# Kernel optimization log

Hardware: AMD Instinct MI355X
Metric: run time of the kernel (lower is better)

The kernel has to match this reference:

```python
import jax, jax.numpy as jnp
import numpy as np

B, N, D, H, M, CD = 2, 2048, 1024, 16, 77, 768
DH = D // H          # head dim 64
FF = 4 * D           # GEGLU hidden 4096
NBITS = 8
EPS = 1e-5


def fake_quant_w(w, n_bits=NBITS):
    """Per-tensor uniform affine INT8 fake-quant (UniformAffineQuantizerINT8) with STE."""
    levels = 2 ** n_bits - 1
    mn = jnp.min(w)
    mx = jnp.max(w)
    delta = (mx - mn) / levels
    zp = jnp.round(-mn / delta)
    wq = jnp.clip(jnp.round(w / delta) + zp, 0, levels)
    wdq = (wq - zp) * delta
    return w + jax.lax.stop_gradient(wdq - w)


def layernorm(x, g, b):
    mu = jnp.mean(x, axis=-1, keepdims=True)
    var = jnp.mean((x - mu) ** 2, axis=-1, keepdims=True)
    return (x - mu) * jax.lax.rsqrt(var + EPS) * g + b


def linear(x, w, b=None):
    y = x @ fake_quant_w(w).T
    return y if b is None else y + b


def cross_attn(x, ctx, qw, kw, vw, ow, ob):
    Bq, Nq, _ = x.shape
    Nk = ctx.shape[1]
    q = linear(x, qw).reshape(Bq, Nq, H, DH)     # b n h d
    k = linear(ctx, kw).reshape(Bq, Nk, H, DH)
    v = linear(ctx, vw).reshape(Bq, Nk, H, DH)
    scale = DH ** -0.5
    sim = jnp.einsum('bihd,bjhd->bhij', q, k) * scale   # [B,H,Nq,Nk]
    attn = jax.nn.softmax(sim, axis=-1)
    out = jnp.einsum('bhij,bjhd->bihd', attn, v).reshape(Bq, Nq, D)
    return linear(out, ow, ob)


def geglu_ff(x, w1, b1, w2, b2):
    h = linear(x, w1, b1)                # [B,N,2*FF]
    hidden, gate = jnp.split(h, 2, axis=-1)
    return linear(hidden * jax.nn.gelu(gate), w2, b2)


def setup_inputs() -> dict:
    key = jax.random.key(0)
    ks = jax.random.split(key, 24)
    W = lambda k, o, i: (jax.random.normal(k, (o, i), jnp.float32) * 0.02)
    return {
        'x': jax.random.normal(ks[0], (B, N, D), jnp.float32),
        'context': jax.random.normal(ks[1], (B, M, CD), jnp.float32),
        'ln1_g': 1.0 + 0.1 * jax.random.normal(ks[2], (D,), jnp.float32),
        'ln1_b': 0.1 * jax.random.normal(ks[3], (D,), jnp.float32),
        'ln2_g': 1.0 + 0.1 * jax.random.normal(ks[4], (D,), jnp.float32),
        'ln2_b': 0.1 * jax.random.normal(ks[5], (D,), jnp.float32),
        'ln3_g': 1.0 + 0.1 * jax.random.normal(ks[6], (D,), jnp.float32),
        'ln3_b': 0.1 * jax.random.normal(ks[7], (D,), jnp.float32),
        'q1_w': W(ks[8], D, D), 'k1_w': W(ks[9], D, D), 'v1_w': W(ks[10], D, D),
        'o1_w': W(ks[11], D, D), 'o1_b': jnp.zeros((D,), jnp.float32),
        'q2_w': W(ks[12], D, D), 'k2_w': W(ks[13], D, CD), 'v2_w': W(ks[14], D, CD),
        'o2_w': W(ks[15], D, D), 'o2_b': jnp.zeros((D,), jnp.float32),
        'ff1_w': W(ks[16], 2 * FF, D), 'ff1_b': jnp.zeros((2 * FF,), jnp.float32),
        'ff2_w': W(ks[17], D, FF), 'ff2_b': jnp.zeros((D,), jnp.float32),
    }


def reference(x, context, ln1_g, ln1_b, ln2_g, ln2_b, ln3_g, ln3_b,
              q1_w, k1_w, v1_w, o1_w, o1_b,
              q2_w, k2_w, v2_w, o2_w, o2_b,
              ff1_w, ff1_b, ff2_w, ff2_b):
    x = cross_attn(layernorm(x, ln1_g, ln1_b), layernorm(x, ln1_g, ln1_b),
                   q1_w, k1_w, v1_w, o1_w, o1_b) + x
    x = cross_attn(layernorm(x, ln2_g, ln2_b), context,
                   q2_w, k2_w, v2_w, o2_w, o2_b) + x
    x = geglu_ff(layernorm(x, ln3_g, ln3_b), ff1_w, ff1_b, ff2_w, ff2_b) + x
    return x
```

## Files before the change

### kernel.cpp

```cpp
#include <hip/hip_runtime.h>
#include <cstdint>
#include <cstddef>

typedef unsigned short ushort_t;
typedef short s16x8 __attribute__((ext_vector_type(8)));
typedef float f32x4 __attribute__((ext_vector_type(4)));
typedef unsigned u32x4 __attribute__((ext_vector_type(4)));

#define MFMA(A,B,C) __builtin_amdgcn_mfma_f32_16x16x32_bf16((A),(B),(C),0,0,0)

__device__ __forceinline__ float b2f(ushort_t h){ return __uint_as_float(((unsigned)h)<<16); }
__device__ __forceinline__ ushort_t f2b(float f){
  unsigned u = __float_as_uint(f);
  u += 0x7FFFu + ((u >> 16) & 1u);
  return (ushort_t)(u >> 16);
}
__device__ __forceinline__ unsigned f2o(float f){
  unsigned u = __float_as_uint(f);
  return (u & 0x80000000u) ? ~u : (u | 0x80000000u);
}
__device__ __forceinline__ float o2f(unsigned u){
  unsigned b = (u & 0x80000000u) ? (u & 0x7FFFFFFFu) : ~u;
  return __uint_as_float(b);
}

struct QT { const float* w[10]; ushort_t* o[10]; int n[10]; float os[10]; int pm[10]; };

__global__ void init_k(unsigned* slots){
  int t = threadIdx.x;
  if (t < 20) slots[t] = (t & 1) ? 0u : 0xFFFFFFFFu;
}

__global__ __launch_bounds__(256) void minmax_k(QT qt, unsigned* slots){
  int t = blockIdx.y;
  const float4* w = (const float4*)qt.w[t];
  int n4 = qt.n[t] >> 2;
  float mn = 3.4e38f, mx = -3.4e38f;
  for (int i = blockIdx.x*256 + threadIdx.x; i < n4; i += gridDim.x*256){
    float4 v = w[i];
    mn = fminf(mn, fminf(fminf(v.x, v.y), fminf(v.z, v.w)));
    mx = fmaxf(mx, fmaxf(fmaxf(v.x, v.y), fmaxf(v.z, v.w)));
  }
  #pragma unroll
  for (int o = 1; o < 64; o <<= 1){
    mn = fminf(mn, __shfl_xor(mn, o));
    mx = fmaxf(mx, __shfl_xor(mx, o));
  }
  __shared__ float smn[4], smx[4];
  int wv = threadIdx.x >> 6;
  if ((threadIdx.x & 63) == 0){ smn[wv] = mn; smx[wv] = mx; }
  __syncthreads();
  if (threadIdx.x == 0){
    mn = fminf(fminf(smn[0], smn[1]), fminf(smn[2], smn[3]));
    mx = fmaxf(fmaxf(smx[0], smx[1]), fmaxf(smx[2], smx[3]));
    atomicMin(&slots[2*t], f2o(mn));
    atomicMax(&slots[2*t+1], f2o(mx));
  }
}

__global__ __launch_bounds__(256) void dequant_k(QT qt, const unsigned* __restrict__ slots){
  int t = blockIdx.y;
  float mn = o2f(slots[2*t]), mx = o2f(slots[2*t+1]);
  float delta = (mx - mn) * (1.f/255.f);
  float zp = rintf(-mn / delta);
  float osc = qt.os[t];
  int pm = qt.pm[t];
  const float4* w = (const float4*)qt.w[t];
  ushort4* o = (ushort4*)qt.o[t];
  int n4 = qt.n[t] >> 2;
  for (int i = blockIdx.x*256 + threadIdx.x; i < n4; i += gridDim.x*256){
    float4 v = w[i];
    ushort4 r;
    float q;
    q = fminf(fmaxf(rintf(v.x/delta) + zp, 0.f), 255.f); r.x = f2b((q - zp)*delta*osc);
    q = fminf(fmaxf(rintf(v.y/delta) + zp, 0.f), 255.f); r.y = f2b((q - zp)*delta*osc);
    q = fminf(fmaxf(rintf(v.z/delta) + zp, 0.f), 255.f); r.z = f2b((q - zp)*delta*osc);
    q = fminf(fmaxf(rintf(v.w/delta) + zp, 0.f), 255.f); r.w = f2b((q - zp)*delta*osc);
    size_t oi = i;
    if (pm){
      int row = i >> 8, c4 = i & 255;
      int nr = (row < 4096) ? ((row >> 5) << 6) + (row & 31)
                            : (((row - 4096) >> 5) << 6) + 32 + ((row - 4096) & 31);
      oi = (size_t)nr*256 + c4;
    }
    o[oi] = r;
  }
}

__global__ __launch_bounds__(256) void f2b_k(const float* __restrict__ in, ushort_t* __restrict__ out, int n4){
  for (int i = blockIdx.x*256 + threadIdx.x; i < n4; i += gridDim.x*256){
    float4 v = ((const float4*)in)[i];
    ushort4 r; r.x = f2b(v.x); r.y = f2b(v.y); r.z = f2b(v.z); r.w = f2b(v.w);
    ((ushort4*)out)[i] = r;
  }
}

__global__ __launch_bounds__(256) void ln_k(const float* __restrict__ x, const float* __restrict__ g,
                                            const float* __restrict__ b, ushort_t* __restrict__ out){
  int row = blockIdx.x, tid = threadIdx.x;
  float4 v = ((const float4*)(x + (size_t)row*1024))[tid];
  float s  = v.x + v.y + v.z + v.w;
  float s2 = v.x*v.x + v.y*v.y + v.z*v.z + v.w*v.w;
  #pragma unroll
  for (int o = 1; o < 64; o <<= 1){ s += __shfl_xor(s, o); s2 += __shfl_xor(s2, o); }
  __shared__ float rs[4], rs2[4];
  int wv = tid >> 6;
  if ((tid & 63) == 0){ rs[wv] = s; rs2[wv] = s2; }
  __syncthreads();
  s = rs[0]+rs[1]+rs[2]+rs[3]; s2 = rs2[0]+rs2[1]+rs2[2]+rs2[3];
  float mu = s * (1.f/1024.f);
  float var = s2 * (1.f/1024.f) - mu*mu;
  float rstd = rsqrtf(var + 1e-5f);
  float4 gv = ((const float4*)g)[tid], bv = ((const float4*)b)[tid];
  ushort4 r;
  r.x = f2b((v.x - mu)*rstd*gv.x + bv.x);
  r.y = f2b((v.y - mu)*rstd*gv.y + bv.y);
  r.z = f2b((v.z - mu)*rstd*gv.z + bv.z);
  r.w = f2b((v.w - mu)*rstd*gv.w + bv.w);
  ((ushort4*)(out + (size_t)row*1024))[tid] = r;
}

__global__ __launch_bounds__(256) void reduce_ln_k(
    const float* __restrict__ p0, const float* __restrict__ p1,
    const float* __restrict__ bias, const float* __restrict__ resid,
    const float* __restrict__ lng, const float* __restrict__ lnb_,
    float* __restrict__ xout, ushort_t* __restrict__ lnout)
{
  int row = blockIdx.x, tid = threadIdx.x;
  size_t bi = (size_t)row*256 + tid;
  float4 a = ((const float4*)p0)[bi];
  float4 b = ((const float4*)p1)[bi];
  float4 r = ((const float4*)resid)[bi];
  float4 bb = ((const float4*)bias)[tid];
  float4 v;
  v.x = a.x + b.x + r.x + bb.x;
  v.y = a.y + b.y + r.y + bb.y;
  v.z = a.z + b.z + r.z + bb.z;
  v.w = a.w + b.w + r.w + bb.w;
  ((float4*)xout)[bi] = v;
  float s  = v.x + v.y + v.z + v.w;
  float s2 = v.x*v.x + v.y*v.y + v.z*v.z + v.w*v.w;
  #pragma unroll
  for (int o = 1; o < 64; o <<= 1){ s += __shfl_xor(s, o); s2 += __shfl_xor(s2, o); }
  __shared__ float rs[4], rs2[4];
  int wv = tid >> 6;
  if ((tid & 63) == 0){ rs[wv] = s; rs2[wv] = s2; }
  __syncthreads();
  s = rs[0]+rs[1]+rs[2]+rs[3]; s2 = rs2[0]+rs2[1]+rs2[2]+rs2[3];
  float mu = s * (1.f/1024.f);
  float var = s2 * (1.f/1024.f) - mu*mu;
  float rstd = rsqrtf(var + 1e-5f);
  float4 gv = ((const float4*)lng)[tid], bv = ((const float4*)lnb_)[tid];
  ushort4 o;
  o.x = f2b((v.x - mu)*rstd*gv.x + bv.x);
  o.y = f2b((v.y - mu)*rstd*gv.y + bv.y);
  o.z = f2b((v.z - mu)*rstd*gv.z + bv.z);
  o.w = f2b((v.w - mu)*rstd*gv.w + bv.w);
  ((ushort4*)(lnout + (size_t)row*1024))[tid] = o;
}

__global__ __launch_bounds__(512) void gemm_k(
    const ushort_t* __restrict__ A, const ushort_t* __restrict__ W,
    const float* __restrict__ bias, const float* __restrict__ resid,
    float* __restrict__ outF, ushort_t* __restrict__ outB,
    int M, int N, int K, int lda, int ldw)
{
  __shared__ ushort_t As[3][256*32];
  __shared__ ushort_t Bs[3][128*32];
  const int tid = threadIdx.x;
  const int lane = tid & 63, wv = tid >> 6;
  const int g = lane >> 4, qi = lane & 15;

  const int gx = gridDim.x, gy = gridDim.y;
  const int lid = blockIdx.x + blockIdx.y * gx;
  int m0, n0;
  if (((gx & 3) | (gy & 1)) == 0){
    const int w = gx >> 2, h = gy >> 1;
    const int xcd = lid & 7, o = lid >> 3;
    const int cx = xcd & 3, cy = xcd >> 2;
    n0 = (cx * w + (o % w)) * 128;
    m0 = (cy * h + (o / w)) * 256;
  } else {
    n0 = blockIdx.x * 128;
    m0 = blockIdx.y * 256;
  }

  const int koff = blockIdx.z * K;
  if (gridDim.z > 1) outF += (size_t)blockIdx.z * M * N;

  const int wr = (wv >> 1) * 64, wc = (wv & 1) * 64;
  f32x4 acc[4][4] = {};

  const int ra0 = tid >> 2,        sa0 = (tid & 3) ^ ((ra0 >> 1) & 3);
  const int ra1 = (512+tid) >> 2,  sa1 = ((512+tid) & 3) ^ ((ra1 >> 1) & 3);
  const int aA0 = (m0 + ra0 < M) ? m0 + ra0 : M - 1;
  const int aA1 = (m0 + ra1 < M) ? m0 + ra1 : M - 1;
  const size_t dA0 = (size_t)tid*8, dA1 = (size_t)(512+tid)*8, dB0 = (size_t)tid*8;

  #define GSTAGE(bi_, kt_) do {                                                    \
    __builtin_amdgcn_global_load_lds(                                              \
      (const __attribute__((address_space(1))) void*)(A + (size_t)aA0*lda + koff + (kt_) + sa0*8), \
      (__attribute__((address_space(3))) void*)(&As[bi_][dA0]), 16, 0, 0);         \
    __builtin_amdgcn_global_load_lds(                                              \
      (const __attribute__((address_space(1))) void*)(A + (size_t)aA1*lda + koff + (kt_) + sa1*8), \
      (__attribute__((address_space(3))) void*)(&As[bi_][dA1]), 16, 0, 0);         \
    __builtin_amdgcn_global_load_lds(                                              \
      (const __attribute__((address_space(1))) void*)(W + (size_t)(n0 + ra0)*ldw + koff + (kt_) + sa0*8), \
      (__attribute__((address_space(3))) void*)(&Bs[bi_][dB0]), 16, 0, 0);         \
  } while(0)

  const int nt = K >> 5;
  GSTAGE(0, 0);
  if (nt > 1) GSTAGE(1, 32);
  if (nt > 1) asm volatile("s_waitcnt vmcnt(3)" ::: "memory");
  else        asm volatile("s_waitcnt vmcnt(0)" ::: "memory");
  __builtin_amdgcn_s_barrier();
  __builtin_amdgcn_sched_barrier(0);

  int bi = 0;
  for (int t = 0; t < nt; ++t){
    int b2 = bi + 2; if (b2 >= 3) b2 -= 3;
    if (t + 2 < nt) GSTAGE(b2, (t + 2) << 5);
    s16x8 af[4], bfr[4];
    #pragma unroll
    for (int mi = 0; mi < 4; ++mi){
      int row = wr + mi*16 + qi;
      int sl = g ^ ((row >> 1) & 3);
      af[mi] = *(const s16x8*)(&As[bi][row*32 + sl*8]);
    }
    #pragma unroll
    for (int ni = 0; ni < 4; ++ni){
      int row = wc + ni*16 + qi;
      int sl = g ^ ((row >> 1) & 3);
      bfr[ni] = *(const s16x8*)(&Bs[bi][row*32 + sl*8]);
    }
    __builtin_amdgcn_s_setprio(1);
    #pragma unroll
    for (int mi = 0; mi < 4; ++mi)
      #pragma unroll
      for (int ni = 0; ni < 4; ++ni)
        acc[mi][ni] = MFMA(af[mi], bfr[ni], acc[mi][ni]);
    __builtin_amdgcn_s_setprio(0);
    if (t + 1 < nt){
      if (t + 2 < nt) asm volatile("s_waitcnt vmcnt(3)" ::: "memory");
      else            asm volatile("s_waitcnt vmcnt(0)" ::: "memory");
      __builtin_amdgcn_s_barrier();
      __builtin_amdgcn_sched_barrier(0);
    }
    bi += 1; if (bi >= 3) bi -= 3;
  }
  #undef GSTAGE

  #pragma unroll
  for (int mi = 0; mi < 4; ++mi){
    #pragma unroll
    for (int r = 0; r < 4; ++r){
      int row = m0 + wr + mi*16 + g*4 + r;
      if (row >= M) continue;
      #pragma unroll
      for (int ni = 0; ni < 4; ++ni){
        int col = n0 + wc + ni*16 + qi;
        float v = acc[mi][ni][r];
        if (bias)  v += bias[col];
        if (resid) v += resid[(size_t)row*N + col];
        if (outF)  outF[(size_t)row*N + col] = v;
        else       outB[(size_t)row*N + col] = f2b(v);
      }
    }
  }
}

__global__ __launch_bounds__(512) void gemm_ff1_k(
    const ushort_t* __restrict__ A, const ushort_t* __restrict__ W,
    const float* __restrict__ biasHG, ushort_t* __restrict__ out)
{
  __shared__ ushort_t As[3][256*32];
  __shared__ ushort_t Bs[3][128*32];
  const int tid = threadIdx.x;
  const int lane = tid & 63, wv = tid >> 6;
  const int g = lane >> 4, qi = lane & 15;
  const int lda = 1024, ldw = 1024;

  const int gx = gridDim.x;
  const int gy = gridDim.y;
  const int lid = blockIdx.x + blockIdx.y * gx;
  const int w = gx >> 2, h = gy >> 1;
  const int xcd = lid & 7, o = lid >> 3;
  const int cx = xcd & 3, cy = xcd >> 2;
  const int n0 = (cx * w + (o % w)) * 128;
  const int m0 = (cy * h + (o / w)) * 256;

  const int wr = (wv >> 1) * 64, wc = (wv & 1) * 64;
  f32x4 acc[4][4] = {};

  const int ra0 = tid >> 2,        sa0 = (tid & 3) ^ ((ra0 >> 1) & 3);
  const int ra1 = (512+tid) >> 2,  sa1 = ((512+tid) & 3) ^ ((ra1 >> 1) & 3);
  const int aA0 = m0 + ra0, aA1 = m0 + ra1;
  const size_t dA0 = (size_t)tid*8, dA1 = (size_t)(512+tid)*8, dB0 = (size_t)tid*8;

  #define GSTAGEF(bi_, kt_) do {                                                   \
    __builtin_amdgcn_global_load_lds(                                              \
      (const __attribute__((address_space(1))) void*)(A + (size_t)aA0*lda + (kt_) + sa0*8), \
      (__attribute__((address_space(3))) void*)(&As[bi_][dA0]), 16, 0, 0);         \
    __builtin_amdgcn_global_load_lds(                                              \
      (const __attribute__((address_space(1))) void*)(A + (size_t)aA1*lda + (kt_) + sa1*8), \
      (__attribute__((address_space(3))) void*)(&As[bi_][dA1]), 16, 0, 0);         \
    __builtin_amdgcn_global_load_lds(                                              \
      (const __attribute__((address_space(1))) void*)(W + (size_t)(n0 + ra0)*ldw + (kt_) + sa0*8), \
      (__attribute__((address_space(3))) void*)(&Bs[bi_][dB0]), 16, 0, 0);         \
  } while(0)

  const int nt = 1024 >> 5;
  GSTAGEF(0, 0);
  GSTAGEF(1, 32);
  asm volatile("s_waitcnt vmcnt(3)" ::: "memory");
  __builtin_amdgcn_s_barrier();
  __builtin_amdgcn_sched_barrier(0);

  int bi = 0;
  for (int t = 0; t < nt; ++t){
    int b2 = bi + 2; if (b2 >= 3) b2 -= 3;
    if (t + 2 < nt) GSTAGEF(b2, (t + 2) << 5);
    s16x8 af[4], bfr[4];
    #pragma unroll
    for (int mi = 0; mi < 4; ++mi){
      int row = wr + mi*16 + qi;
      int sl = g ^ ((row >> 1) & 3);
      af[mi] = *(const s16x8*)(&As[bi][row*32 + sl*8]);
    }
    #pragma unroll
    for (int ni = 0; ni < 4; ++ni){
      int row = wc + ni*16 + qi;
      int sl = g ^ ((row >> 1) & 3);
      bfr[ni] = *(const s16x8*)(&Bs[bi][row*32 + sl*8]);
    }
    __builtin_amdgcn_s_setprio(1);
    #pragma unroll
    for (int mi = 0; mi < 4; ++mi)
      #pragma unroll
      for (int ni = 0; ni < 4; ++ni)
        acc[mi][ni] = MFMA(af[mi], bfr[ni], acc[mi][ni]);
    __builtin_amdgcn_s_setprio(0);
    if (t + 1 < nt){
      if (t + 2 < nt) asm volatile("s_waitcnt vmcnt(3)" ::: "memory");
      else            asm volatile("s_waitcnt vmcnt(0)" ::: "memory");
      __builtin_amdgcn_s_barrier();
      __builtin_amdgcn_sched_barrier(0);
    }
    bi += 1; if (bi >= 3) bi -= 3;
  }
  #undef GSTAGEF

  const int jw = (n0 + wc) >> 1;
  #pragma unroll
  for (int mi = 0; mi < 4; ++mi){
    #pragma unroll
    for (int r = 0; r < 4; ++r){
      int row = m0 + wr + mi*16 + g*4 + r;
      #pragma unroll
      for (int ni = 0; ni < 2; ++ni){
        int j = jw + ni*16 + qi;
        float hv = acc[mi][ni][r]   + biasHG[j];
        float gg = acc[mi][ni+2][r] + biasHG[4096 + j];
        float tt = 0.7978845608f*(gg + 0.044715f*gg*gg*gg);
        float e  = __builtin_amdgcn_exp2f(2.885390082f*tt);
        float th = 1.f - 2.f/(e + 1.f);
        float ge = 0.5f*gg*(1.f + th);
        out[(size_t)row*4096 + j] = f2b(hv * ge);
      }
    }
  }
}

__global__ __launch_bounds__(256) void reduce_k(const float* __restrict__ p0, const float* __restrict__ p1,
                                                const float* __restrict__ bias, const float* __restrict__ resid,
                                                float* __restrict__ outF, ushort_t* __restrict__ outB, int n4){
  for (int i = blockIdx.x*256 + threadIdx.x; i < n4; i += gridDim.x*256){
    float4 a = ((const float4*)p0)[i];
    float4 b = ((const float4*)p1)[i];
    float4 v;
    v.x = a.x + b.x; v.y = a.y + b.y; v.z = a.z + b.z; v.w = a.w + b.w;
    if (bias){
      float4 bb = ((const float4*)bias)[i & 255];
      v.x += bb.x; v.y += bb.y; v.z += bb.z; v.w += bb.w;
    }
    if (resid){
      float4 r = ((const float4*)resid)[i];
      v.x += r.x; v.y += r.y; v.z += r.z; v.w += r.w;
    }
    if (outF) ((float4*)outF)[i] = v;
    else {
      ushort4 o; o.x = f2b(v.x); o.y = f2b(v.y); o.z = f2b(v.z); o.w = f2b(v.w);
      ((ushort4*)outB)[i] = o;
    }
  }
}

__global__ __launch_bounds__(256) void reduce4_k(const float* __restrict__ p0, const float* __restrict__ p1,
                                                 const float* __restrict__ p2, const float* __restrict__ p3,
                                                 const float* __restrict__ bias, const float* __restrict__ resid,
                                                 float* __restrict__ outF, int n4){
  for (int i = blockIdx.x*256 + threadIdx.x; i < n4; i += gridDim.x*256){
    float4 a = ((const float4*)p0)[i];
    float4 b = ((const float4*)p1)[i];
    float4 c = ((const float4*)p2)[i];
    float4 d = ((const float4*)p3)[i];
    float4 r = ((const float4*)resid)[i];
    float4 bb = ((const float4*)bias)[i & 255];
    float4 v;
    v.x = (a.x + b.x) + (c.x + d.x) + r.x + bb.x;
    v.y = (a.y + b.y) + (c.y + d.y) + r.y + bb.y;
    v.z = (a.z + b.z) + (c.z + d.z) + r.z + bb.z;
    v.w = (a.w + b.w) + (c.w + d.w) + r.w + bb.w;
    ((float4*)outF)[i] = v;
  }
}

__global__ __launch_bounds__(256) void vtrans_k(const ushort_t* __restrict__ src, ushort_t* __restrict__ dst,
                                                int rows, int stride, int col_off, int nk_pad){
  __shared__ ushort_t ldst[64*130];
  int n0 = blockIdx.x * 128;
  int b = blockIdx.y >> 4, h = blockIdx.y & 15;
  const ushort_t* s = src + (size_t)b*rows*stride + col_off + h*64;
  for (int idx = threadIdx.x; idx < 128*64; idx += 256){
    int n = idx >> 6, d = idx & 63;
    int ng = n0 + n;
    ushort_t v = (ng < rows) ? s[(size_t)ng*stride + d] : (ushort_t)0;
    ldst[d*130 + n] = v;
  }
  __syncthreads();
  ushort_t* o = dst + (size_t)(b*16 + h)*64*nk_pad;
  for (int idx = threadIdx.x; idx < 64*128; idx += 256){
    int d = idx >> 7, n = idx & 127;
    if (n0 + n < nk_pad) o[(size_t)d*nk_pad + n0 + n] = ldst[d*130 + n];
  }
}

__global__ __launch_bounds__(512) void attn_k(
    const ushort_t* __restrict__ Q, const ushort_t* __restrict__ Kp, const ushort_t* __restrict__ Vt,
    ushort_t* __restrict__ O, int nq, int nk, int qstride, int kvstride, int nk_pad)
{
  __shared__ ushort_t Ks[2][32*64];
  __shared__ ushort_t Vs[2][64*32];
  const int tid = threadIdx.x, lane = tid & 63, wv = tid >> 6;
  const int g = lane >> 4, qi = lane & 15;
  const int b = blockIdx.y >> 4, h = blockIdx.y & 15;
  const int q0 = blockIdx.x*128 + wv*16;

  const ushort_t* Qr = Q + (size_t)(b*nq + q0 + qi)*qstride + h*64;
  s16x8 qf0 = *(const s16x8*)(Qr + g*8);
  s16x8 qf1 = *(const s16x8*)(Qr + 32 + g*8);
  const ushort_t* Kb = Kp + (size_t)b*nk*kvstride + h*64;
  const ushort_t* Vb = Vt + (size_t)(b*16 + h)*64*nk_pad;

  const int krow = (wv & 3)*8 + (lane >> 3);
  const int kgsl = (lane & 7) ^ (krow & 7);
  const int vrow = (wv & 3)*16 + (lane >> 2);
  const int vgsl = (lane & 3) ^ ((vrow >> 1) & 3);

  #define STAGE(buf, kb_) do {                                                   \
    if (wv < 4){                                                                 \
      int kr_ = (kb_) + krow; if (kr_ >= nk) kr_ = nk - 1;                       \
      __builtin_amdgcn_global_load_lds(                                          \
        (const __attribute__((address_space(1))) void*)(Kb + (size_t)kr_*kvstride + kgsl*8), \
        (__attribute__((address_space(3))) void*)(&Ks[buf][(size_t)(wv&3)*512]), 16, 0, 0); \
    } else {                                                                     \
      __builtin_amdgcn_global_load_lds(                                          \
        (const __attribute__((address_space(1))) void*)(Vb + (size_t)vrow*nk_pad + (kb_) + vgsl*8), \
        (__attribute__((address_space(3))) void*)(&Vs[buf][(size_t)(wv&3)*512]), 16, 0, 0); \
    }                                                                            \
  } while(0)

  const int nkp = (nk + 31) & ~31;
  f32x4 ot[4] = {};
  float m_run = -1e30f, lsum = 0.f;

  const int ks0 = (g     ^ (qi & 7)) * 8;
  const int ks1 = ((4+g) ^ (qi & 7)) * 8;
  const int vs0 = (g ^ ((qi >> 1) & 3)) * 8;

  STAGE(0, 0);
  asm volatile("s_waitcnt vmcnt(0)" ::: "memory");
  __syncthreads();
  int cur = 0;
  for (int kb = 0; kb < nkp; kb += 32){
    if (kb + 32 < nkp) STAGE(cur^1, kb + 32);
    s16x8 ka0 = *(const s16x8*)(&Ks[cur][(qi)*64      + ks0]);
    s16x8 ka1 = *(const s16x8*)(&Ks[cur][(qi)*64      + ks1]);
    s16x8 kb0 = *(const s16x8*)(&Ks[cur][(16+qi)*64   + ks0]);
    s16x8 kb1 = *(const s16x8*)(&Ks[cur][(16+qi)*64   + ks1]);
    s16x8 vf0 = *(const s16x8*)(&Vs[cur][(qi)*32      + vs0]);
    s16x8 vf1 = *(const s16x8*)(&Vs[cur][(16+qi)*32   + vs0]);
    s16x8 vf2 = *(const s16x8*)(&Vs[cur][(32+qi)*32   + vs0]);
    s16x8 vf3 = *(const s16x8*)(&Vs[cur][(48+qi)*32   + vs0]);

    f32x4 st0 = {}, st1 = {};
    __builtin_amdgcn_s_setprio(1);
    st0 = MFMA(ka0, qf0, st0);
    st0 = MFMA(ka1, qf1, st0);
    st1 = MFMA(kb0, qf0, st1);
    st1 = MFMA(kb1, qf1, st1);
    __builtin_amdgcn_s_setprio(0);
    float s[8];
    #pragma unroll
    for (int r = 0; r < 4; ++r){ s[r] = st0[r]; s[4+r] = st1[r]; }
    if (kb + 32 > nk){
      #pragma unroll
      for (int r = 0; r < 4; ++r){
        if (kb + 4*g + r >= nk)      s[r]   = -1e30f;
        if (kb + 16 + 4*g + r >= nk) s[4+r] = -1e30f;
      }
    }
    float m1 = fmaxf(fmaxf(s[0], s[1]), s[2]);
    float m2 = fmaxf(fmaxf(s[3], s[4]), s[5]);
    float bm = fmaxf(fmaxf(m1, m2), fmaxf(s[6], s[7]));
    bm = fmaxf(bm, __shfl_xor(bm, 16));
    bm = fmaxf(bm, __shfl_xor(bm, 32));
    if (!__all(bm <= m_run)){
      float m_new = fmaxf(m_run, bm);
      float fac = __builtin_amdgcn_exp2f(m_run - m_new);
      lsum *= fac;
      #pragma unroll
      for (int dd = 0; dd < 4; ++dd)
        #pragma unroll
        for (int r = 0; r < 4; ++r) ot[dd][r] *= fac;
      m_run = m_new;
    }
    float p[8], ps = 0.f;
    #pragma unroll
    for (int i = 0; i < 8; ++i){ p[i] = __builtin_amdgcn_exp2f(s[i] - m_run); ps += p[i]; }
    lsum += ps;
    unsigned pk[4];
    #pragma unroll
    for (int r = 0; r < 4; ++r)
      asm("v_cvt_pk_bf16_f32 %0, %1, %2" : "=v"(pk[r]) : "v"(p[r]), "v"(p[4+r]));
    int srcbase = ((2*g) & 3) * 16 + qi;
    unsigned sh0[4], sh1[4];
    #pragma unroll
    for (int r = 0; r < 4; ++r){
      sh0[r] = (unsigned)__shfl((int)pk[r], srcbase);
      sh1[r] = (unsigned)__shfl((int)pk[r], srcbase + 16);
    }
    unsigned sel = (g >> 1) ? 0x07060302u : 0x05040100u;
    u32x4 pw;
    pw[0] = __builtin_amdgcn_perm(sh0[1], sh0[0], sel);
    pw[1] = __builtin_amdgcn_perm(sh0[3], sh0[2], sel);
    pw[2] = __builtin_amdgcn_perm(sh1[1], sh1[0], sel);
    pw[3] = __builtin_amdgcn_perm(sh1[3], sh1[2], sel);
    s16x8 pf = __builtin_bit_cast(s16x8, pw);
    __builtin_amdgcn_s_setprio(1);
    ot[0] = MFMA(vf0, pf, ot[0]);
    ot[1] = MFMA(vf1, pf, ot[1]);
    ot[2] = MFMA(vf2, pf, ot[2]);
    ot[3] = MFMA(vf3, pf, ot[3]);
    __builtin_amdgcn_s_setprio(0);

    asm volatile("s_waitcnt vmcnt(0)" ::: "memory");
    __syncthreads();
    cur ^= 1;
  }
  #undef STAGE
  float l = lsum;
  l += __shfl_xor(l, 16);
  l += __shfl_xor(l, 32);
  float inv = 1.f / l;
  ushort_t* Or = O + (size_t)(b*nq + q0 + qi)*1024 + h*64;
  #pragma unroll
  for (int dd = 0; dd < 4; ++dd)
    #pragma unroll
    for (int r = 0; r < 4; ++r)
      Or[dd*16 + 4*g + r] = f2b(ot[dd][r] * inv);
}

extern "C" void kernel_launch(void* const* d_in, const int* in_sizes, int n_in,
                              void* d_out, int out_size, void* d_ws, size_t ws_size,
                              hipStream_t stream)
{
  const float* x    = (const float*)d_in[0];
  const float* ctx  = (const float*)d_in[1];
  const float* ln1g = (const float*)d_in[2];
  const float* ln1b = (const float*)d_in[3];
  const float* ln2g = (const float*)d_in[4];
  const float* ln2b = (const float*)d_in[5];
  const float* ln3g = (const float*)d_in[6];
  const float* ln3b = (const float*)d_in[7];
  const float* q1w  = (const float*)d_in[8];
  const float* k1w  = (const float*)d_in[9];
  const float* v1w  = (const float*)d_in[10];
  const float* o1w  = (const float*)d_in[11];
  const float* o1b  = (const float*)d_in[12];
  const float* q2w  = (const float*)d_in[13];
  const float* k2w  = (const float*)d_in[14];
  const float* v2w  = (const float*)d_in[15];
  const float* o2w  = (const float*)d_in[16];
  const float* o2b  = (const float*)d_in[17];
  const float* ff1w = (const float*)d_in[18];
  const float* ff1b = (const float*)d_in[19];
  const float* ff2w = (const float*)d_in[20];
  const float* ff2b = (const float*)d_in[21];

  char* base = (char*)d_ws;
  size_t off = 0;
  auto alloc = [&](size_t bytes) -> char* {
    char* p = base + off;
    off += (bytes + 255) & ~(size_t)255;
    return p;
  };
  unsigned*  slots = (unsigned*)alloc(80);
  ushort_t*  ctxb  = (ushort_t*)alloc((size_t)154*768*2);
  ushort_t*  wqkv1 = (ushort_t*)alloc((size_t)3072*1024*2);
  ushort_t*  o1d   = (ushort_t*)alloc((size_t)1024*1024*2);
  ushort_t*  q2d   = (ushort_t*)alloc((size_t)1024*1024*2);
  ushort_t*  wkv2  = (ushort_t*)alloc((size_t)2048*768*2);
  ushort_t*  o2d   = (ushort_t*)alloc((size_t)1024*1024*2);
  ushort_t*  f1d   = (ushort_t*)alloc((size_t)8192*1024*2);
  ushort_t*  f2d   = (ushort_t*)alloc((size_t)1024*4096*2);
  ushort_t*  lnb   = (ushort_t*)alloc((size_t)4096*1024*2);
  ushort_t*  qkvb  = (ushort_t*)alloc((size_t)4096*3072*2);
  ushort_t*  q2b   = (ushort_t*)alloc((size_t)4096*1024*2);
  ushort_t*  atb   = (ushort_t*)alloc((size_t)4096*1024*2);
  ushort_t*  kvb   = (ushort_t*)alloc((size_t)154*2048*2);
  ushort_t*  vt1   = (ushort_t*)alloc((size_t)2*16*64*2048*2);
  ushort_t*  vt2   = (ushort_t*)alloc((size_t)2*16*64*96*2);
  float*     x1    = (float*)alloc((size_t)4096*1024*4);
  float*     x2    = (float*)alloc((size_t)4096*1024*4);
  ushort_t*  hb    = (ushort_t*)alloc((size_t)4096*8192*2);
  ushort_t*  actb  = qkvb;
  float*     part  = (float*)hb;
  float*     part1 = part + (size_t)4096*1024;
  float*     part2 = part + (size_t)2*4096*1024;
  float*     part3 = part + (size_t)3*4096*1024;

  const float SC = 0.18033688011f;
  QT qt;
  qt.w[0]=q1w;  qt.o[0]=wqkv1;               qt.n[0]=1024*1024; qt.os[0]=SC;  qt.pm[0]=0;
  qt.w[1]=k1w;  qt.o[1]=wqkv1+1024*1024;     qt.n[1]=1024*1024; qt.os[1]=1.f; qt.pm[1]=0;
  qt.w[2]=v1w;  qt.o[2]=wqkv1+2*1024*1024;   qt.n[2]=1024*1024; qt.os[2]=1.f; qt.pm[2]=0;
  qt.w[3]=o1w;  qt.o[3]=o1d;                 qt.n[3]=1024*1024; qt.os[3]=1.f; qt.pm[3]=0;
  qt.w[4]=q2w;  qt.o[4]=q2d;                 qt.n[4]=1024*1024; qt.os[4]=SC;  qt.pm[4]=0;
  qt.w[5]=k2w;  qt.o[5]=wkv2;                qt.n[5]=1024*768;  qt.os[5]=1.f; qt.pm[5]=0;
  qt.w[6]=v2w;  qt.o[6]=wkv2+1024*768;       qt.n[6]=1024*768;  qt.os[6]=1.f; qt.pm[6]=0;
  qt.w[7]=o2w;  qt.o[7]=o2d;                 qt.n[7]=1024*1024; qt.os[7]=1.f; qt.pm[7]=0;
  qt.w[8]=ff1w; qt.o[8]=f1d;                 qt.n[8]=8192*1024; qt.os[8]=1.f; qt.pm[8]=1;
  qt.w[9]=ff2w; qt.o[9]=f2d;                 qt.n[9]=1024*4096; qt.os[9]=1.f; qt.pm[9]=0;

  init_k<<<1, 64, 0, stream>>>(slots);
  minmax_k<<<dim3(256,10), 256, 0, stream>>>(qt, slots);
  dequant_k<<<dim3(256,10), 256, 0, stream>>>(qt, slots);
  f2b_k<<<64, 256, 0, stream>>>(ctx, ctxb, 154*768/4);

  ln_k<<<4096, 256, 0, stream>>>(x, ln1g, ln1b, lnb);
  gemm_k<<<dim3(24, 16), 512, 0, stream>>>(lnb, wqkv1, nullptr, nullptr,
                                           nullptr, qkvb, 4096, 3072, 1024, 1024, 1024);
  vtrans_k<<<dim3(16, 32), 256, 0, stream>>>(qkvb, vt1, 2048, 3072, 2048, 2048);
  attn_k<<<dim3(16, 32), 512, 0, stream>>>(qkvb, qkvb+1024, vt1, atb,
                                           2048, 2048, 3072, 3072, 2048);
  gemm_k<<<dim3(8, 16, 2), 512, 0, stream>>>(atb, o1d, nullptr, nullptr,
                                             part, nullptr, 4096, 1024, 512, 1024, 1024);
  reduce_ln_k<<<4096, 256, 0, stream>>>(part, part1, o1b, x, ln2g, ln2b, x1, lnb);

  gemm_k<<<dim3(8, 16, 2), 512, 0, stream>>>(lnb, q2d, nullptr, nullptr,
                                             part, nullptr, 4096, 1024, 512, 1024, 1024);
  reduce_k<<<2048, 256, 0, stream>>>(part, part1, nullptr, nullptr, nullptr, q2b, 4096*1024/4);
  gemm_k<<<dim3(16, 1), 512, 0, stream>>>(ctxb, wkv2, nullptr, nullptr,
                                          nullptr, kvb, 154, 2048, 768, 768, 768);
  vtrans_k<<<dim3(1, 32), 256, 0, stream>>>(kvb, vt2, 77, 2048, 1024, 96);
  attn_k<<<dim3(16, 32), 512, 0, stream>>>(q2b, kvb, vt2, atb,
                                           2048, 77, 1024, 2048, 96);
  gemm_k<<<dim3(8, 16, 2), 512, 0, stream>>>(atb, o2d, nullptr, nullptr,
                                             part, nullptr, 4096, 1024, 512, 1024, 1024);
  reduce_ln_k<<<4096, 256, 0, stream>>>(part, part1, o2b, x1, ln3g, ln3b, x2, lnb);

  gemm_ff1_k<<<dim3(64, 16), 512, 0, stream>>>(lnb, f1d, ff1b, actb);
  gemm_k<<<dim3(8, 16, 4), 512, 0, stream>>>(actb, f2d, nullptr, nullptr,
                                             part, nullptr, 4096, 1024, 1024, 4096, 4096);
  reduce4_k<<<2048, 256, 0, stream>>>(part, part1, part2, part3, ff2b, x2,
                                      (float*)d_out, 4096*1024/4);
}
```

Measured before the change: 527.3 us.

## Split self-attention along keys into two halves with a merge kernel

```diff
diff --git a/kernel.cpp b/kernel.cpp
--- a/kernel.cpp
+++ b/kernel.cpp
@@ -416,6 +416,31 @@
   }
 }
 
+__global__ __launch_bounds__(256) void attnmerge_k(
+    const float* __restrict__ Ou, const float* __restrict__ ml,
+    ushort_t* __restrict__ O)
+{
+  int row = blockIdx.x, t = threadIdx.x;
+  int q = row & 2047, b = row >> 11, h = t >> 4;
+  size_t mli = ((size_t)(b*16 + h))*2048 + q;
+  const float2* mlp = (const float2*)ml;
+  float2 ml0 = mlp[mli];
+  float2 ml1 = mlp[(size_t)32*2048 + mli];
+  float m = fmaxf(ml0.x, ml1.x);
+  float w0 = __builtin_amdgcn_exp2f(ml0.x - m);
+  float w1 = __builtin_amdgcn_exp2f(ml1.x - m);
+  float inv = 1.f / (w0*ml0.y + w1*ml1.y);
+  size_t oi = (size_t)row*256 + t;
+  float4 a = ((const float4*)Ou)[oi];
+  float4 c = ((const float4*)Ou)[(size_t)4096*256 + oi];
+  ushort4 r;
+  r.x = f2b((w0*a.x + w1*c.x)*inv);
+  r.y = f2b((w0*a.y + w1*c.y)*inv);
+  r.z = f2b((w0*a.z + w1*c.z)*inv);
+  r.w = f2b((w0*a.w + w1*c.w)*inv);
+  ((ushort4*)O)[oi] = r;
+}
+
 __global__ __launch_bounds__(256) void vtrans_k(const ushort_t* __restrict__ src, ushort_t* __restrict__ dst,
                                                 int rows, int stride, int col_off, int nk_pad){
   __shared__ ushort_t ldst[64*130];
@@ -438,7 +463,8 @@
 
 __global__ __launch_bounds__(512) void attn_k(
     const ushort_t* __restrict__ Q, const ushort_t* __restrict__ Kp, const ushort_t* __restrict__ Vt,
-    ushort_t* __restrict__ O, int nq, int nk, int qstride, int kvstride, int nk_pad)
+    ushort_t* __restrict__ O, int nq, int nk, int qstride, int kvstride, int nk_pad,
+    int nkz, float* __restrict__ OuF, float* __restrict__ ml)
 {
   __shared__ ushort_t Ks[2][32*64];
   __shared__ ushort_t Vs[2][64*32];
@@ -446,6 +472,7 @@
   const int g = lane >> 4, qi = lane & 15;
   const int b = blockIdx.y >> 4, h = blockIdx.y & 15;
   const int q0 = blockIdx.x*128 + wv*16;
+  const int z = blockIdx.z;
 
   const ushort_t* Qr = Q + (size_t)(b*nq + q0 + qi)*qstride + h*64;
   s16x8 qf0 = *(const s16x8*)(Qr + g*8);
@@ -471,7 +498,9 @@
     }                                                                            \
   } while(0)
 
-  const int nkp = (nk + 31) & ~31;
+  const int kb0 = (OuF ? z * nkz : 0);
+  const int kbend0 = (OuF ? (kb0 + nkz) : nk);
+  const int kbend = (kbend0 + 31) & ~31;
   f32x4 ot[4] = {};
   float m_run = -1e30f, lsum = 0.f;
 
@@ -479,16 +508,16 @@
   const int ks1 = ((4+g) ^ (qi & 7)) * 8;
   const int vs0 = (g ^ ((qi >> 1) & 3)) * 8;
 
-  STAGE(0, 0);
+  STAGE(0, kb0);
   asm volatile("s_waitcnt vmcnt(0)" ::: "memory");
   __syncthreads();
   int cur = 0;
-  for (int kb = 0; kb < nkp; kb += 32){
-    if (kb + 32 < nkp) STAGE(cur^1, kb + 32);
+  for (int kb = kb0; kb < kbend; kb += 32){
+    if (kb + 32 < kbend) STAGE(cur^1, kb + 32);
     s16x8 ka0 = *(const s16x8*)(&Ks[cur][(qi)*64      + ks0]);
     s16x8 ka1 = *(const s16x8*)(&Ks[cur][(qi)*64      + ks1]);
-    s16x8 kb0 = *(const s16x8*)(&Ks[cur][(16+qi)*64   + ks0]);
-    s16x8 kb1 = *(const s16x8*)(&Ks[cur][(16+qi)*64   + ks1]);
+    s16x8 kb0f = *(const s16x8*)(&Ks[cur][(16+qi)*64  + ks0]);
+    s16x8 kb1f = *(const s16x8*)(&Ks[cur][(16+qi)*64  + ks1]);
     s16x8 vf0 = *(const s16x8*)(&Vs[cur][(qi)*32      + vs0]);
     s16x8 vf1 = *(const s16x8*)(&Vs[cur][(16+qi)*32   + vs0]);
     s16x8 vf2 = *(const s16x8*)(&Vs[cur][(32+qi)*32   + vs0]);
@@ -498,8 +527,8 @@
     __builtin_amdgcn_s_setprio(1);
     st0 = MFMA(ka0, qf0, st0);
     st0 = MFMA(ka1, qf1, st0);
-    st1 = MFMA(kb0, qf0, st1);
-    st1 = MFMA(kb1, qf1, st1);
+    st1 = MFMA(kb0f, qf0, st1);
+    st1 = MFMA(kb1f, qf1, st1);
     __builtin_amdgcn_s_setprio(0);
     float s[8];
     #pragma unroll
@@ -563,13 +592,26 @@
   float l = lsum;
   l += __shfl_xor(l, 16);
   l += __shfl_xor(l, 32);
-  float inv = 1.f / l;
-  ushort_t* Or = O + (size_t)(b*nq + q0 + qi)*1024 + h*64;
-  #pragma unroll
-  for (int dd = 0; dd < 4; ++dd)
-    #pragma unroll
-    for (int r = 0; r < 4; ++r)
-      Or[dd*16 + 4*g + r] = f2b(ot[dd][r] * inv);
+  if (OuF){
+    float* Or = OuF + (size_t)z*4096*1024 + (size_t)(b*nq + q0 + qi)*1024 + h*64;
+    #pragma unroll
+    for (int dd = 0; dd < 4; ++dd)
+      #pragma unroll
+      for (int r = 0; r < 4; ++r)
+        Or[dd*16 + 4*g + r] = ot[dd][r];
+    if (g == 0){
+      float2* mlp = (float2*)ml;
+      mlp[((size_t)(z*2 + b)*16 + h)*2048 + (q0 + qi)] = make_float2(m_run, l);
+    }
+  } else {
+    float inv = 1.f / l;
+    ushort_t* Or = O + (size_t)(b*nq + q0 + qi)*1024 + h*64;
+    #pragma unroll
+    for (int dd = 0; dd < 4; ++dd)
+      #pragma unroll
+      for (int r = 0; r < 4; ++r)
+        Or[dd*16 + 4*g + r] = f2b(ot[dd][r] * inv);
+  }
 }
 
 extern "C" void kernel_launch(void* const* d_in, const int* in_sizes, int n_in,
@@ -622,6 +664,7 @@
   ushort_t*  kvb   = (ushort_t*)alloc((size_t)154*2048*2);
   ushort_t*  vt1   = (ushort_t*)alloc((size_t)2*16*64*2048*2);
   ushort_t*  vt2   = (ushort_t*)alloc((size_t)2*16*64*96*2);
+  float*     mlbuf = (float*)alloc((size_t)2*2*16*2048*8);
   float*     x1    = (float*)alloc((size_t)4096*1024*4);
   float*     x2    = (float*)alloc((size_t)4096*1024*4);
   ushort_t*  hb    = (ushort_t*)alloc((size_t)4096*8192*2);
@@ -653,8 +696,10 @@
   gemm_k<<<dim3(24, 16), 512, 0, stream>>>(lnb, wqkv1, nullptr, nullptr,
                                            nullptr, qkvb, 4096, 3072, 1024, 1024, 1024);
   vtrans_k<<<dim3(16, 32), 256, 0, stream>>>(qkvb, vt1, 2048, 3072, 2048, 2048);
-  attn_k<<<dim3(16, 32), 512, 0, stream>>>(qkvb, qkvb+1024, vt1, atb,
-                                           2048, 2048, 3072, 3072, 2048);
+  attn_k<<<dim3(16, 32, 2), 512, 0, stream>>>(qkvb, qkvb+1024, vt1, nullptr,
+                                              2048, 2048, 3072, 3072, 2048,
+                                              1024, part, mlbuf);
+  attnmerge_k<<<4096, 256, 0, stream>>>(part, mlbuf, atb);
   gemm_k<<<dim3(8, 16, 2), 512, 0, stream>>>(atb, o1d, nullptr, nullptr,
                                              part, nullptr, 4096, 1024, 512, 1024, 1024);
   reduce_ln_k<<<4096, 256, 0, stream>>>(part, part1, o1b, x, ln2g, ln2b, x1, lnb);
@@ -665,8 +710,9 @@
   gemm_k<<<dim3(16, 1), 512, 0, stream>>>(ctxb, wkv2, nullptr, nullptr,
                                           nullptr, kvb, 154, 2048, 768, 768, 768);
   vtrans_k<<<dim3(1, 32), 256, 0, stream>>>(kvb, vt2, 77, 2048, 1024, 96);
-  attn_k<<<dim3(16, 32), 512, 0, stream>>>(q2b, kvb, vt2, atb,
-                                           2048, 77, 1024, 2048, 96);
+  attn_k<<<dim3(16, 32, 1), 512, 0, stream>>>(q2b, kvb, vt2, atb,
+                                              2048, 77, 1024, 2048, 96,
+                                              0, nullptr, nullptr);
   gemm_k<<<dim3(8, 16, 2), 512, 0, stream>>>(atb, o2d, nullptr, nullptr,
                                              part, nullptr, 4096, 1024, 512, 1024, 1024);
   reduce_ln_k<<<4096, 256, 0, stream>>>(part, part1, o2b, x1, ln3g, ln3b, x2, lnb);
```

Measured after the change: 541.8 us. 2.8% more time.
